# Optimization experiments

Hardware: AMD Instinct MI355X
Metric: run time of the kernel (lower is better)

## Reference

```python
import jax, jax.numpy as jnp
import numpy as np

D_MODEL, D_STATE, EXPAND, HEADDIM = 768, 64, 2, 64
D_INNER = EXPAND * D_MODEL            # 1536
NHEADS = D_INNER // HEADDIM           # 24
D_IN_PROJ = 2 * D_INNER + 2 * D_STATE + 2 * NHEADS  # 3248
DT_MIN, DT_MAX, DT_INIT_FLOOR, A_FLOOR = 1e-3, 1e-1, 1e-4, 1e-4
LN_EPS = 1e-5


def setup_inputs() -> dict:
    key = jax.random.key(0)
    ks = jax.random.split(key, 8)
    B, L = 2, 1024
    u = jax.random.normal(ks[0], (B, L, D_MODEL), dtype=jnp.float32)
    s_in = 1.0 / np.sqrt(D_MODEL)
    s_out = 1.0 / np.sqrt(D_INNER)
    Win = jax.random.uniform(ks[1], (D_IN_PROJ, D_MODEL), jnp.float32, -s_in, s_in)
    Wout = jax.random.uniform(ks[2], (D_MODEL, D_INNER), jnp.float32, -s_out, s_out)
    _dt = jnp.clip(jnp.exp(jax.random.uniform(ks[3], (NHEADS,)) * (np.log(DT_MAX) - np.log(DT_MIN)) + np.log(DT_MIN)), DT_INIT_FLOOR, None)
    dt_bias = _dt + jnp.log(-jnp.expm1(-_dt))
    D = jnp.ones((NHEADS,), jnp.float32)
    Bg = jnp.ones((D_STATE,), jnp.float32)
    Bb = jnp.zeros((D_STATE,), jnp.float32)
    Cg = jnp.ones((D_STATE,), jnp.float32)
    Cb = jnp.zeros((D_STATE,), jnp.float32)
    return {"u": u, "Win": Win, "Wout": Wout, "dt_bias": dt_bias, "D": D,
            "Bg": Bg, "Bb": Bb, "Cg": Cg, "Cb": Cb}


def _layernorm(x, g, b):
    m = jnp.mean(x, axis=-1, keepdims=True)
    v = jnp.var(x, axis=-1, keepdims=True)
    return (x - m) * jax.lax.rsqrt(v + LN_EPS) * g + b


def reference(u, Win, Wout, dt_bias, D, Bg, Bb, Cg, Cb):
    B_, L, _ = u.shape
    nH, hD, dS = NHEADS, HEADDIM, D_STATE
    proj = u @ Win.T  # (B, L, D_IN_PROJ)
    z, x, Bp, Cp, dd_dt, dd_A = jnp.split(
        proj, np.cumsum([D_INNER, D_INNER, dS, dS, nH])[:-0 or None], axis=-1) if False else (
        proj[..., :D_INNER],
        proj[..., D_INNER:2 * D_INNER],
        proj[..., 2 * D_INNER:2 * D_INNER + dS],
        proj[..., 2 * D_INNER + dS:2 * D_INNER + 2 * dS],
        proj[..., 2 * D_INNER + 2 * dS:2 * D_INNER + 2 * dS + nH],
        proj[..., 2 * D_INNER + 2 * dS + nH:])
    x = x.reshape(B_, L, nH, hD)
    z = z.reshape(B_, L, nH, hD)
    Bn = _layernorm(Bp, Bg, Bb)  # (B, L, dS), shared across heads
    Cn = _layernorm(Cp, Cg, Cb)
    DT = jax.nn.softplus(dd_dt + dt_bias)                    # (B, L, nH)
    A = jnp.minimum(-jax.nn.softplus(dd_A), -A_FLOOR)        # (B, L, nH)
    dec = jnp.exp(A * DT)                                    # (B, L, nH)

    def step(h, inp):
        x_t, Bn_t, Cn_t, DT_t, dec_t = inp
        upd = jnp.einsum('bhp,bn->bhpn', x_t, Bn_t) * DT_t[..., None, None]
        h = dec_t[..., None, None] * h + upd
        y_t = jnp.einsum('bhpn,bn->bhp', h, Cn_t) + D[None, :, None] * x_t
        return h, y_t

    h0 = jnp.zeros((B_, nH, hD, dS), u.dtype)
    xs = (jnp.swapaxes(x, 0, 1), jnp.swapaxes(Bn, 0, 1), jnp.swapaxes(Cn, 0, 1),
          jnp.swapaxes(DT, 0, 1), jnp.swapaxes(dec, 0, 1))
    _, ys = jax.lax.scan(step, h0, xs)            # ys: (L, B, nH, hD)
    y = jnp.swapaxes(ys, 0, 1) * jax.nn.silu(z)   # (B, L, nH, hD)
    y = y.reshape(B_, L, D_INNER)
    return y @ Wout.T
```

## Files before the change

kernel.cpp:

```cpp
#include <hip/hip_runtime.h>
#include <cstdint>

#define D_MODEL   768
#define D_STATE   64
#define D_INNER   1536
#define NHEADS    24
#define HEADDIM   64
#define D_PROJ    3248
#define BATCH     2
#define SEQ       1024
#define ROWS      (BATCH*SEQ)
#define LN_EPS    1e-5f
#define A_FLOOR   1e-4f
#define QC        64
#define NCH       (SEQ/QC)
#define LSTR      72

#define RG_U    32
#define RG_WIN  52
#define RG_WO   12
#define KT_1    24
#define KT_2    48

typedef __attribute__((ext_vector_type(8))) short short8;
typedef __attribute__((ext_vector_type(4))) float f32x4;

__device__ __forceinline__ unsigned short f2bf(float f) {
  union { float f; uint32_t u; } v; v.f = f;
  uint32_t r = (v.u + 0x7FFFu + ((v.u >> 16) & 1u)) >> 16;
  return (unsigned short)r;
}
__device__ __forceinline__ float bf2f(unsigned short u) {
  union { uint32_t u; float f; } v; v.u = (uint32_t)u << 16;
  return v.f;
}
__device__ __forceinline__ void storeC(float v, float* p) { *p = v; }
__device__ __forceinline__ void storeC(float v, unsigned short* p) { *p = f2bf(v); }

__device__ __forceinline__ void gload_lds16(const void* g, void* l) {
  __builtin_amdgcn_global_load_lds(
      (const __attribute__((address_space(1))) unsigned int*)g,
      (__attribute__((address_space(3))) unsigned int*)l, 16, 0, 0);
}

template <int N>
__device__ __forceinline__ void wait_vm() {
  static_assert(N == 0 || N == 2 || N == 3 || N == 4 || N == 6 || N == 8,
                "unsupported vmcnt");
  if constexpr (N == 0) asm volatile("s_waitcnt vmcnt(0)" ::: "memory");
  else if constexpr (N == 2) asm volatile("s_waitcnt vmcnt(2)" ::: "memory");
  else if constexpr (N == 3) asm volatile("s_waitcnt vmcnt(3)" ::: "memory");
  else if constexpr (N == 4) asm volatile("s_waitcnt vmcnt(4)" ::: "memory");
  else if constexpr (N == 6) asm volatile("s_waitcnt vmcnt(6)" ::: "memory");
  else if constexpr (N == 8) asm volatile("s_waitcnt vmcnt(8)" ::: "memory");
}

__global__ __launch_bounds__(256) void pack_all_kernel(
    const float* __restrict__ u, const float* __restrict__ Win,
    const float* __restrict__ Wout, unsigned short* __restrict__ upk,
    unsigned short* __restrict__ Winpk, unsigned short* __restrict__ Wopk) {
  int b = blockIdx.x;
  const float* src; unsigned short* dst; int K, RG, kt, rg, srcRows;
  if (b < KT_1 * RG_U) {
    src = u; dst = upk; K = 768; RG = RG_U; kt = b / RG_U; rg = b % RG_U; srcRows = ROWS;
  } else if (b < KT_1 * RG_U + KT_1 * RG_WIN) {
    int i = b - KT_1 * RG_U;
    src = Win; dst = Winpk; K = 768; RG = RG_WIN; kt = i / RG_WIN; rg = i % RG_WIN; srcRows = D_PROJ;
  } else {
    int i = b - KT_1 * RG_U - KT_1 * RG_WIN;
    src = Wout; dst = Wopk; K = 1536; RG = RG_WO; kt = i / RG_WO; rg = i % RG_WO; srcRows = D_MODEL;
  }
  const int t = threadIdx.x;
  const int lr = t >> 2, cq = t & 3;
  const int R = rg * 64 + lr;
  float4 v0 = make_float4(0.f, 0.f, 0.f, 0.f), v1 = v0;
  if (R < srcRows) {
    const float* p = src + (size_t)R * K + kt * 32 + cq * 8;
    v0 = *(const float4*)p;
    v1 = *(const float4*)(p + 4);
  }
  ushort4 oa, ob;
  oa.x = f2bf(v0.x); oa.y = f2bf(v0.y); oa.z = f2bf(v0.z); oa.w = f2bf(v0.w);
  ob.x = f2bf(v1.x); ob.y = f2bf(v1.y); ob.z = f2bf(v1.z); ob.w = f2bf(v1.w);
  unsigned short* o = dst + ((size_t)(kt * RG + rg) * 4 + cq) * 512 + lr * 8;
  *(ushort4*)o = oa;
  *(ushort4*)(o + 4) = ob;
}

template <int TBM, int TBN, int GX, int GY, bool XMAJOR, int SPLIT, typename CT>
__global__ __launch_bounds__(256 * SPLIT) void gemm_bt_bf16(
    const unsigned short* __restrict__ A, const unsigned short* __restrict__ B,
    CT* __restrict__ C, int aRG, int bRG, int M, int N, int K) {
  constexpr int MF = TBM / 32;
  constexpr int NF = TBN / 32;
  constexpr int NSA = TBM / 16;
  constexpr int NSB = TBN / 16;
  constexpr int LPW = (NSA + NSB) / 4;
  static_assert((NSA + NSB) % 4 == 0, "segments must split evenly over waves");
  constexpr int NWG = GX * GY;
  constexpr int PER = NWG / 8;
  static_assert(NWG % 8 == 0, "grid must split evenly over 8 XCDs");
  __shared__ unsigned short Asm[SPLIT][3][TBM * 32];
  __shared__ unsigned short Bsm[SPLIT][3][TBN * 32];

  const int tid = threadIdx.x;
  const int w = tid >> 6, lane = tid & 63;
  const int khalf = w >> 2;
  const int wv = w & 3;
  const int kTiles = (K / SPLIT) >> 5;
  const int ktBase = khalf * kTiles;

  const int g = (blockIdx.x & 7) * PER + (blockIdx.x >> 3);
  int bx, by;
  if constexpr (XMAJOR) { by = g / GX; bx = g - by * GX; }
  else                  { bx = g / GY; by = g - bx * GY; }
  const int bm = by * TBM, bn = bx * TBN;

  const int wm = (wv & 1) * (TBM / 2);
  const int wn = (wv >> 1) * (TBN / 2);
  const int gq = lane >> 4, r = lane & 15;

  f32x4 acc[MF][NF];
#pragma unroll
  for (int i = 0; i < MF; ++i)
#pragma unroll
    for (int j = 0; j < NF; ++j) acc[i][j] = (f32x4){0.f, 0.f, 0.f, 0.f};

  auto stage = [&](int t, int buf) {
    const int kt = ktBase + t;
    for (int s = wv; s < NSA + NSB; s += 4) {
      if (s < NSA) {
        const unsigned short* src =
            A + ((size_t)kt * aRG + (bm >> 6) + (s >> 2)) * 2048 + (s & 3) * 512 + lane * 8;
        gload_lds16(src, (void*)(&Asm[khalf][buf][s * 512]));
      } else {
        int s2 = s - NSA;
        const unsigned short* src =
            B + ((size_t)kt * bRG + (bn >> 6) + (s2 >> 2)) * 2048 + (s2 & 3) * 512 + lane * 8;
        gload_lds16(src, (void*)(&Bsm[khalf][buf][s2 * 512]));
      }
    }
  };

  stage(0, 0);
  stage(1, 1);

  int cur = 0;
  for (int t = 0; t < kTiles; ++t) {
    if (t + 1 < kTiles) wait_vm<LPW>();
    else                wait_vm<0>();
    __builtin_amdgcn_s_barrier();
    asm volatile("" ::: "memory");

    if (t + 2 < kTiles) stage(t + 2, (t + 2) % 3);

    short8 a[MF], b[NF];
#pragma unroll
    for (int mf = 0; mf < MF; ++mf) {
      int ra = wm + mf * 16 + r;
      a[mf] = *(const short8*)&Asm[khalf][cur][(ra >> 6) * 2048 + gq * 512 + (ra & 63) * 8];
    }
#pragma unroll
    for (int nf = 0; nf < NF; ++nf) {
      int rb = wn + nf * 16 + r;
      b[nf] = *(const short8*)&Bsm[khalf][cur][(rb >> 6) * 2048 + gq * 512 + (rb & 63) * 8];
    }
#pragma unroll
    for (int mf = 0; mf < MF; ++mf)
#pragma unroll
      for (int nf = 0; nf < NF; ++nf)
        acc[mf][nf] = __builtin_amdgcn_mfma_f32_16x16x32_bf16(a[mf], b[nf], acc[mf][nf], 0, 0, 0);

    cur = (cur + 1) % 3;
  }

  if constexpr (SPLIT == 2) {
    __syncthreads();
    float* red = (float*)&Asm[0][0][0];
    if (khalf == 1) {
#pragma unroll
      for (int mf = 0; mf < MF; ++mf)
#pragma unroll
        for (int nf = 0; nf < NF; ++nf)
#pragma unroll
          for (int q = 0; q < 4; ++q)
            red[(size_t)wv * 1024 + ((mf * NF + nf) * 4 + q) * 64 + lane] = acc[mf][nf][q];
    }
    __syncthreads();
    if (khalf == 1) return;
#pragma unroll
    for (int mf = 0; mf < MF; ++mf)
#pragma unroll
      for (int nf = 0; nf < NF; ++nf)
#pragma unroll
        for (int q = 0; q < 4; ++q)
          acc[mf][nf][q] += red[(size_t)wv * 1024 + ((mf * NF + nf) * 4 + q) * 64 + lane];
  }

#pragma unroll
  for (int mf = 0; mf < MF; ++mf) {
#pragma unroll
    for (int nf = 0; nf < NF; ++nf) {
      int col = bn + wn + nf * 16 + r;
      if (col < N) {
#pragma unroll
        for (int q = 0; q < 4; ++q) {
          int row = bm + wm + mf * 16 + gq * 4 + q;
          storeC(acc[mf][nf][q], &C[(size_t)row * N + col]);
        }
      }
    }
  }
}

__device__ __forceinline__ float softplusf(float x) {
  return (x > 20.f) ? x : log1pf(expf(x));
}
__device__ __forceinline__ float wave_sum64(float v) {
#pragma unroll
  for (int o = 32; o > 0; o >>= 1) v += __shfl_xor(v, o);
  return v;
}

__global__ __launch_bounds__(256) void prep_kernel(
    const unsigned short* __restrict__ proj, const float* __restrict__ dt_bias,
    const float* __restrict__ Bg, const float* __restrict__ Bb,
    const float* __restrict__ Cg, const float* __restrict__ Cb,
    unsigned short* __restrict__ BC, float2* __restrict__ aDT) {
  const int r = blockIdx.x * 4 + (threadIdx.x >> 6);
  const int lane = threadIdx.x & 63;
  const unsigned short* p = proj + (size_t)r * D_PROJ;

  float bp = bf2f(p[2 * D_INNER + lane]);
  float cp = bf2f(p[2 * D_INNER + D_STATE + lane]);

  float mb = wave_sum64(bp) * (1.f / 64.f);
  float mc = wave_sum64(cp) * (1.f / 64.f);
  float db = bp - mb, dc = cp - mc;
  float vb = wave_sum64(db * db) * (1.f / 64.f);
  float vc = wave_sum64(dc * dc) * (1.f / 64.f);
  float bn = db * rsqrtf(vb + LN_EPS) * Bg[lane] + Bb[lane];
  float cn = dc * rsqrtf(vc + LN_EPS) * Cg[lane] + Cb[lane];
  BC[(size_t)r * 128 + lane]      = f2bf(bn);
  BC[(size_t)r * 128 + 64 + lane] = f2bf(cn);

  if (lane < NHEADS) {
    float ddt = bf2f(p[2 * D_INNER + 2 * D_STATE + lane]);
    float dA  = bf2f(p[2 * D_INNER + 2 * D_STATE + NHEADS + lane]);
    float DT = softplusf(ddt + dt_bias[lane]);
    float Aa = fminf(-softplusf(dA), -A_FLOOR);
    int b = r >> 10;
    int t = r & 1023;
    aDT[((size_t)(b * NHEADS + lane) << 10) + t] = make_float2(Aa * DT, DT);
  }
}

__device__ __forceinline__ float wave_prefix_incl(float v, int lane) {
#pragma unroll
  for (int o = 1; o < 64; o <<= 1) {
    float w = __shfl_up(v, o);
    if (lane >= o) v += w;
  }
  return v;
}

__global__ __launch_bounds__(256) void chunk_state_kernel(
    const unsigned short* __restrict__ proj, const unsigned short* __restrict__ BC,
    const float2* __restrict__ aDT, float* __restrict__ Tbuf,
    float* __restrict__ Ebuf) {
  const int blk = blockIdx.x;
  const int c = blk & (NCH - 1), bh = blk >> 4;
  const int b = bh / NHEADS, hh = bh % NHEADS;
  const int tid = threadIdx.x;

  __shared__ unsigned short BT[64 * LSTR];
  __shared__ unsigned short XT[64 * LSTR];
  __shared__ float coeff[QC];
  __shared__ float etot[1];

  if (tid < 64) {
    float2 ad = aDT[((size_t)bh << 10) + c * QC + tid];
    float cs = wave_prefix_incl(ad.x, tid);
    float tot = __shfl(cs, 63);
    coeff[tid] = ad.y * __expf(tot - cs);
    if (tid == 63) etot[0] = __expf(tot);
  }
  __syncthreads();

  for (int i = tid; i < 1024; i += 256) {
    int s = i >> 4;
    int q = (i & 15) * 4;
    int r = b * SEQ + c * QC + s;
    ushort4 bv = *(const ushort4*)(BC + (size_t)r * 128 + q);
    ushort4 xv = *(const ushort4*)(proj + (size_t)r * D_PROJ + D_INNER + hh * 64 + q);
    float cf = coeff[s];
    BT[(q + 0) * LSTR + s] = bv.x;
    BT[(q + 1) * LSTR + s] = bv.y;
    BT[(q + 2) * LSTR + s] = bv.z;
    BT[(q + 3) * LSTR + s] = bv.w;
    XT[(q + 0) * LSTR + s] = f2bf(bf2f(xv.x) * cf);
    XT[(q + 1) * LSTR + s] = f2bf(bf2f(xv.y) * cf);
    XT[(q + 2) * LSTR + s] = f2bf(bf2f(xv.z) * cf);
    XT[(q + 3) * LSTR + s] = f2bf(bf2f(xv.w) * cf);
  }
  __syncthreads();

  const int w = tid >> 6, l = tid & 63;
  const int r16 = l & 15, g = l >> 4;
  f32x4 acc[4];
#pragma unroll
  for (int i = 0; i < 4; ++i) acc[i] = (f32x4){0.f, 0.f, 0.f, 0.f};

#pragma unroll
  for (int kk = 0; kk < 2; ++kk) {
    short8 a = *(const short8*)&BT[(w * 16 + r16) * LSTR + kk * 32 + g * 8];
#pragma unroll
    for (int pf = 0; pf < 4; ++pf) {
      short8 bf = *(const short8*)&XT[(pf * 16 + r16) * LSTR + kk * 32 + g * 8];
      acc[pf] = __builtin_amdgcn_mfma_f32_16x16x32_bf16(a, bf, acc[pf], 0, 0, 0);
    }
  }

  float* T = Tbuf + (size_t)blk * 4096;
#pragma unroll
  for (int pf = 0; pf < 4; ++pf)
#pragma unroll
    for (int q = 0; q < 4; ++q)
      T[(size_t)(w * 16 + g * 4 + q) * 64 + pf * 16 + r16] = acc[pf][q];
  if (tid == 0) Ebuf[blk] = etot[0];
}

__global__ __launch_bounds__(256) void interchunk_kernel(
    const float* __restrict__ Tbuf, const float* __restrict__ Ebuf,
    float* __restrict__ Sinbuf) {
  const int bh = blockIdx.x >> 2, part = blockIdx.x & 3;
  const int tid = threadIdx.x;
  const size_t eo = (size_t)part * 1024 + tid * 4;
  float4 s = make_float4(0.f, 0.f, 0.f, 0.f);
#pragma unroll
  for (int c = 0; c < NCH; ++c) {
    size_t off = ((size_t)(bh * NCH + c)) * 4096 + eo;
    *(float4*)(Sinbuf + off) = s;
    float E = Ebuf[bh * NCH + c];
    float4 t4 = *(const float4*)(Tbuf + off);
    s.x = fmaf(E, s.x, t4.x);
    s.y = fmaf(E, s.y, t4.y);
    s.z = fmaf(E, s.z, t4.z);
    s.w = fmaf(E, s.w, t4.w);
  }
}

__global__ __launch_bounds__(256) void chunk_output_kernel(
    const unsigned short* __restrict__ proj, const unsigned short* __restrict__ BC,
    const float2* __restrict__ aDT, const float* __restrict__ Sinbuf,
    const float* __restrict__ Dv, unsigned short* __restrict__ Ybf) {
  const int blk = blockIdx.x;
  const int c = blk & (NCH - 1), bh = blk >> 4;
  const int b = bh / NHEADS, hh = bh % NHEADS;
  const int tid = threadIdx.x;

  __shared__ unsigned short Cc[64 * LSTR];
  __shared__ unsigned short Bc[64 * LSTR];
  __shared__ unsigned short SinT[64 * LSTR];
  __shared__ unsigned short XT[64 * LSTR];
  __shared__ unsigned short Wl[64 * LSTR];
  __shared__ float csum[QC];
  __shared__ float DTs[QC];

  if (tid < 64) {
    float2 ad = aDT[((size_t)bh << 10) + c * QC + tid];
    csum[tid] = wave_prefix_incl(ad.x, tid);
    DTs[tid] = ad.y;
  }

  const size_t sin_base = (size_t)blk * 4096;
  for (int i = tid; i < 1024; i += 256) {
    int s = i >> 4;
    int q = (i & 15) * 4;
    int r = b * SEQ + c * QC + s;
    ushort4 bv = *(const ushort4*)(BC + (size_t)r * 128 + q);
    ushort4 cv = *(const ushort4*)(BC + (size_t)r * 128 + 64 + q);
    ushort4 xv = *(const ushort4*)(proj + (size_t)r * D_PROJ + D_INNER + hh * 64 + q);
    float4 sv = *(const float4*)(Sinbuf + sin_base + (size_t)s * 64 + q);
    *(ushort4*)&Cc[s * LSTR + q] = cv;
    *(ushort4*)&Bc[s * LSTR + q] = bv;
    XT[(q + 0) * LSTR + s] = xv.x;
    XT[(q + 1) * LSTR + s] = xv.y;
    XT[(q + 2) * LSTR + s] = xv.z;
    XT[(q + 3) * LSTR + s] = xv.w;
    SinT[(q + 0) * LSTR + s] = f2bf(sv.x);
    SinT[(q + 1) * LSTR + s] = f2bf(sv.y);
    SinT[(q + 2) * LSTR + s] = f2bf(sv.z);
    SinT[(q + 3) * LSTR + s] = f2bf(sv.w);
  }
  __syncthreads();

  const int w = tid >> 6, l = tid & 63;
  const int r16 = l & 15, g = l >> 4;

  f32x4 accg[4], accy[4];
#pragma unroll
  for (int i = 0; i < 4; ++i) {
    accg[i] = (f32x4){0.f, 0.f, 0.f, 0.f};
    accy[i] = (f32x4){0.f, 0.f, 0.f, 0.f};
  }

#pragma unroll
  for (int kk = 0; kk < 2; ++kk) {
    short8 a = *(const short8*)&Cc[(w * 16 + r16) * LSTR + kk * 32 + g * 8];
#pragma unroll
    for (int f = 0; f < 4; ++f) {
      short8 bf = *(const short8*)&Bc[(f * 16 + r16) * LSTR + kk * 32 + g * 8];
      accg[f] = __builtin_amdgcn_mfma_f32_16x16x32_bf16(a, bf, accg[f], 0, 0, 0);
    }
#pragma unroll
    for (int f = 0; f < 4; ++f) {
      short8 bf = *(const short8*)&SinT[(f * 16 + r16) * LSTR + kk * 32 + g * 8];
      accy[f] = __builtin_amdgcn_mfma_f32_16x16x32_bf16(a, bf, accy[f], 0, 0, 0);
    }
  }

  float cst[4], dsc[4];
#pragma unroll
  for (int q = 0; q < 4; ++q) {
    cst[q] = csum[w * 16 + g * 4 + q];
    dsc[q] = __expf(cst[q]);
  }
#pragma unroll
  for (int sf = 0; sf < 4; ++sf) {
    int s = sf * 16 + r16;
    float cs_s = csum[s], dt_s = DTs[s];
#pragma unroll
    for (int q = 0; q < 4; ++q) {
      int t = w * 16 + g * 4 + q;
      float wv = (s <= t) ? accg[sf][q] * __expf(cst[q] - cs_s) * dt_s : 0.f;
      Wl[t * LSTR + s] = f2bf(wv);
    }
  }
#pragma unroll
  for (int f = 0; f < 4; ++f)
#pragma unroll
    for (int q = 0; q < 4; ++q) accy[f][q] *= dsc[q];
  __syncthreads();

#pragma unroll
  for (int kk = 0; kk < 2; ++kk) {
    short8 a = *(const short8*)&Wl[(w * 16 + r16) * LSTR + kk * 32 + g * 8];
#pragma unroll
    for (int f = 0; f < 4; ++f) {
      short8 bf = *(const short8*)&XT[(f * 16 + r16) * LSTR + kk * 32 + g * 8];
      accy[f] = __builtin_amdgcn_mfma_f32_16x16x32_bf16(a, bf, accy[f], 0, 0, 0);
    }
  }

  const float Dh = Dv[hh];
  const int rg = b * 16 + c;
#pragma unroll
  for (int pf = 0; pf < 4; ++pf) {
    int p = pf * 16 + r16;
    int col = hh * 64 + p;
    int kt = col >> 5;
    int cseg = (col >> 3) & 3;
    int jj = p & 7;
    size_t base = ((size_t)(kt * RG_U + rg) * 4 + cseg) * 512 + jj;
#pragma unroll
    for (int q = 0; q < 4; ++q) {
      int t = w * 16 + g * 4 + q;
      int rr = b * SEQ + c * QC + t;
      float x = bf2f(proj[(size_t)rr * D_PROJ + D_INNER + hh * 64 + p]);
      float z = bf2f(proj[(size_t)rr * D_PROJ + hh * 64 + p]);
      float y = accy[pf][q] + Dh * x;
      Ybf[base + (size_t)t * 8] = f2bf(y * (z / (1.f + __expf(-z))));
    }
  }
}

extern "C" void kernel_launch(void* const* d_in, const int* in_sizes, int n_in,
                              void* d_out, int out_size, void* d_ws, size_t ws_size,
                              hipStream_t stream) {
  const float* u       = (const float*)d_in[0];
  const float* Win     = (const float*)d_in[1];
  const float* Wout    = (const float*)d_in[2];
  const float* dt_bias = (const float*)d_in[3];
  const float* Dv      = (const float*)d_in[4];
  const float* Bg      = (const float*)d_in[5];
  const float* Bb      = (const float*)d_in[6];
  const float* Cg      = (const float*)d_in[7];
  const float* Cb      = (const float*)d_in[8];
  float* out = (float*)d_out;

  float* ws = (float*)d_ws;
  unsigned short* projsh = (unsigned short*)ws;
  float*  after_proj = ws + (size_t)ROWS * D_PROJ / 2;
  unsigned short* BCsh = (unsigned short*)after_proj;
  float*  aDTf    = after_proj + (size_t)ROWS * 128 / 2;
  float2* aDT     = (float2*)aDTf;
  float*  Tbuf    = aDTf + (size_t)2 * BATCH * NHEADS * SEQ;
  float*  Ebuf    = Tbuf + (size_t)BATCH * NHEADS * NCH * 4096;
  float*  Sinbuf  = Ebuf + 1024;
  float*  Woutbff = Sinbuf + (size_t)BATCH * NHEADS * NCH * 4096;

  unsigned short* upk   = (unsigned short*)Sinbuf;
  unsigned short* Winpk = (unsigned short*)Tbuf;
  unsigned short* Ypk   = (unsigned short*)Tbuf;
  unsigned short* Wopk  = (unsigned short*)Woutbff;

  pack_all_kernel<<<KT_1 * RG_U + KT_1 * RG_WIN + KT_2 * RG_WO, 256, 0, stream>>>(
      u, Win, Wout, upk, Winpk, Wopk);

  gemm_bt_bf16<128, 128, 26, 16, false, 1, unsigned short><<<416, 256, 0, stream>>>(
      upk, Winpk, projsh, RG_U, RG_WIN, ROWS, D_PROJ, D_MODEL);

  prep_kernel<<<ROWS / 4, 256, 0, stream>>>(projsh, dt_bias, Bg, Bb, Cg, Cb, BCsh, aDT);

  chunk_state_kernel<<<BATCH * NHEADS * NCH, 256, 0, stream>>>(projsh, BCsh, aDT, Tbuf, Ebuf);
  interchunk_kernel<<<BATCH * NHEADS * 4, 256, 0, stream>>>(Tbuf, Ebuf, Sinbuf);
  chunk_output_kernel<<<BATCH * NHEADS * NCH, 256, 0, stream>>>(projsh, BCsh, aDT, Sinbuf, Dv, Ypk);

  gemm_bt_bf16<64, 64, 12, 32, true, 2, float><<<384, 512, 0, stream>>>(
      Ypk, Wopk, out, RG_U, RG_WO, ROWS, D_MODEL, D_INNER);
}
```

Measured before the change: 78.57 us.

## Fuse LayerNorm into GEMM epilogue and merge chunk-state with inter-chunk scan

The B/C LayerNorm moves into the epilogue of the input-projection GEMM, and the separate prep kernel is removed. Chunk-state and inter-chunk kernels merge into one kernel per (batch, head, quarter of headdim) that loops sequentially over chunks, keeps the running state in registers, and prefetches the next chunk's inputs. DT and decay are recomputed from proj in both scan kernels instead of being stored, which removes several launches and intermediate buffers (Tbuf, Ebuf, aDT). In exchange the fused scan runs only 192 blocks with a serial loop over chunks, which lowers parallelism, and the LN uses a single-pass variance.

```diff
diff --git a/kernel.cpp b/kernel.cpp
--- a/kernel.cpp
+++ b/kernel.cpp
@@ -15,6 +15,8 @@
 #define QC        64
 #define NCH       (SEQ/QC)
 #define LSTR      72
+#define COL_DT    3200
+#define COL_DA    3224
 
 #define RG_U    32
 #define RG_WIN  52
@@ -53,6 +55,18 @@
   else if constexpr (N == 4) asm volatile("s_waitcnt vmcnt(4)" ::: "memory");
   else if constexpr (N == 6) asm volatile("s_waitcnt vmcnt(6)" ::: "memory");
   else if constexpr (N == 8) asm volatile("s_waitcnt vmcnt(8)" ::: "memory");
+}
+
+__device__ __forceinline__ float softplusf(float x) {
+  return (x > 20.f) ? x : log1pf(expf(x));
+}
+__device__ __forceinline__ float wave_prefix_incl(float v, int lane) {
+#pragma unroll
+  for (int o = 1; o < 64; o <<= 1) {
+    float w = __shfl_up(v, o);
+    if (lane >= o) v += w;
+  }
+  return v;
 }
 
 __global__ __launch_bounds__(256) void pack_all_kernel(
@@ -87,10 +101,14 @@
   *(ushort4*)(o + 4) = ob;
 }
 
-template <int TBM, int TBN, int GX, int GY, bool XMAJOR, int SPLIT, typename CT>
+template <int TBM, int TBN, int GX, int GY, bool XMAJOR, int SPLIT, bool EPILN,
+          typename CT>
 __global__ __launch_bounds__(256 * SPLIT) void gemm_bt_bf16(
     const unsigned short* __restrict__ A, const unsigned short* __restrict__ B,
-    CT* __restrict__ C, int aRG, int bRG, int M, int N, int K) {
+    CT* __restrict__ C, int aRG, int bRG, int M, int N, int K,
+    const float* __restrict__ LNg0, const float* __restrict__ LNb0,
+    const float* __restrict__ LNg1, const float* __restrict__ LNb1,
+    unsigned short* __restrict__ BCout) {
   constexpr int MF = TBM / 32;
   constexpr int NF = TBN / 32;
   constexpr int NSA = TBM / 16;
@@ -211,148 +229,137 @@
       }
     }
   }
-}
-
-__device__ __forceinline__ float softplusf(float x) {
-  return (x > 20.f) ? x : log1pf(expf(x));
-}
-__device__ __forceinline__ float wave_sum64(float v) {
-#pragma unroll
-  for (int o = 32; o > 0; o >>= 1) v += __shfl_xor(v, o);
-  return v;
-}
-
-__global__ __launch_bounds__(256) void prep_kernel(
-    const unsigned short* __restrict__ proj, const float* __restrict__ dt_bias,
-    const float* __restrict__ Bg, const float* __restrict__ Bb,
-    const float* __restrict__ Cg, const float* __restrict__ Cb,
-    unsigned short* __restrict__ BC, float2* __restrict__ aDT) {
-  const int r = blockIdx.x * 4 + (threadIdx.x >> 6);
-  const int lane = threadIdx.x & 63;
-  const unsigned short* p = proj + (size_t)r * D_PROJ;
-
-  float bp = bf2f(p[2 * D_INNER + lane]);
-  float cp = bf2f(p[2 * D_INNER + D_STATE + lane]);
-
-  float mb = wave_sum64(bp) * (1.f / 64.f);
-  float mc = wave_sum64(cp) * (1.f / 64.f);
-  float db = bp - mb, dc = cp - mc;
-  float vb = wave_sum64(db * db) * (1.f / 64.f);
-  float vc = wave_sum64(dc * dc) * (1.f / 64.f);
-  float bn = db * rsqrtf(vb + LN_EPS) * Bg[lane] + Bb[lane];
-  float cn = dc * rsqrtf(vc + LN_EPS) * Cg[lane] + Cb[lane];
-  BC[(size_t)r * 128 + lane]      = f2bf(bn);
-  BC[(size_t)r * 128 + 64 + lane] = f2bf(cn);
-
-  if (lane < NHEADS) {
-    float ddt = bf2f(p[2 * D_INNER + 2 * D_STATE + lane]);
-    float dA  = bf2f(p[2 * D_INNER + 2 * D_STATE + NHEADS + lane]);
-    float DT = softplusf(ddt + dt_bias[lane]);
-    float Aa = fminf(-softplusf(dA), -A_FLOOR);
-    int b = r >> 10;
-    int t = r & 1023;
-    aDT[((size_t)(b * NHEADS + lane) << 10) + t] = make_float2(Aa * DT, DT);
-  }
-}
-
-__device__ __forceinline__ float wave_prefix_incl(float v, int lane) {
-#pragma unroll
-  for (int o = 1; o < 64; o <<= 1) {
-    float w = __shfl_up(v, o);
-    if (lane >= o) v += w;
-  }
-  return v;
-}
-
-__global__ __launch_bounds__(256) void chunk_state_kernel(
+
+  if constexpr (EPILN) {
+    if (bn == 2 * D_INNER) {
+      const float* gma = (wn == 0) ? LNg0 : LNg1;
+      const float* bta = (wn == 0) ? LNb0 : LNb1;
+      const int half = (wn == 0) ? 0 : 64;
+#pragma unroll
+      for (int mf = 0; mf < MF; ++mf) {
+#pragma unroll
+        for (int q = 0; q < 4; ++q) {
+          float s1 = 0.f, s2 = 0.f;
+#pragma unroll
+          for (int nf = 0; nf < NF; ++nf) {
+            float v = acc[mf][nf][q];
+            s1 += v; s2 += v * v;
+          }
+#pragma unroll
+          for (int o = 1; o < 16; o <<= 1) {
+            s1 += __shfl_xor(s1, o);
+            s2 += __shfl_xor(s2, o);
+          }
+          float mean = s1 * (1.f / 64.f);
+          float var = s2 * (1.f / 64.f) - mean * mean;
+          float rs = rsqrtf(fmaxf(var, 0.f) + LN_EPS);
+          int row = bm + wm + mf * 16 + gq * 4 + q;
+#pragma unroll
+          for (int nf = 0; nf < NF; ++nf) {
+            int n = nf * 16 + r;
+            BCout[(size_t)row * 128 + half + n] =
+                f2bf((acc[mf][nf][q] - mean) * rs * gma[n] + bta[n]);
+          }
+        }
+      }
+    }
+  }
+}
+
+__global__ __launch_bounds__(256) void scan_fused_kernel(
     const unsigned short* __restrict__ proj, const unsigned short* __restrict__ BC,
-    const float2* __restrict__ aDT, float* __restrict__ Tbuf,
-    float* __restrict__ Ebuf) {
-  const int blk = blockIdx.x;
-  const int c = blk & (NCH - 1), bh = blk >> 4;
+    const float* __restrict__ dt_bias, float* __restrict__ Sinbuf) {
+  const int part = blockIdx.x & 3, bh = blockIdx.x >> 2;
   const int b = bh / NHEADS, hh = bh % NHEADS;
+  const int p0 = part * 16;
   const int tid = threadIdx.x;
+  const int w = tid >> 6, l = tid & 63, r16 = l & 15, g = l >> 4;
 
   __shared__ unsigned short BT[64 * LSTR];
-  __shared__ unsigned short XT[64 * LSTR];
-  __shared__ float coeff[QC];
-  __shared__ float etot[1];
-
-  if (tid < 64) {
-    float2 ad = aDT[((size_t)bh << 10) + c * QC + tid];
-    float cs = wave_prefix_incl(ad.x, tid);
-    float tot = __shfl(cs, 63);
-    coeff[tid] = ad.y * __expf(tot - cs);
-    if (tid == 63) etot[0] = __expf(tot);
+  __shared__ unsigned short XT[16 * LSTR];
+  __shared__ float coeffA[NCH][QC];
+  __shared__ float etotA[NCH];
+
+  {
+    const float dtb = dt_bias[hh];
+#pragma unroll
+    for (int j = 0; j < 4; ++j) {
+      int c = w + j * 4;
+      int rr = b * SEQ + c * QC + l;
+      float ddt = bf2f(proj[(size_t)rr * D_PROJ + COL_DT + hh]);
+      float dA  = bf2f(proj[(size_t)rr * D_PROJ + COL_DA + hh]);
+      float DT = softplusf(ddt + dtb);
+      float Aa = fminf(-softplusf(dA), -A_FLOOR);
+      float cs = wave_prefix_incl(Aa * DT, l);
+      float tot = __shfl(cs, 63);
+      coeffA[c][l] = DT * __expf(tot - cs);
+      if (l == 63) etotA[c] = __expf(tot);
+    }
   }
   __syncthreads();
 
-  for (int i = tid; i < 1024; i += 256) {
-    int s = i >> 4;
-    int q = (i & 15) * 4;
-    int r = b * SEQ + c * QC + s;
-    ushort4 bv = *(const ushort4*)(BC + (size_t)r * 128 + q);
-    ushort4 xv = *(const ushort4*)(proj + (size_t)r * D_PROJ + D_INNER + hh * 64 + q);
-    float cf = coeff[s];
-    BT[(q + 0) * LSTR + s] = bv.x;
-    BT[(q + 1) * LSTR + s] = bv.y;
-    BT[(q + 2) * LSTR + s] = bv.z;
-    BT[(q + 3) * LSTR + s] = bv.w;
-    XT[(q + 0) * LSTR + s] = f2bf(bf2f(xv.x) * cf);
-    XT[(q + 1) * LSTR + s] = f2bf(bf2f(xv.y) * cf);
-    XT[(q + 2) * LSTR + s] = f2bf(bf2f(xv.z) * cf);
-    XT[(q + 3) * LSTR + s] = f2bf(bf2f(xv.w) * cf);
-  }
-  __syncthreads();
-
-  const int w = tid >> 6, l = tid & 63;
-  const int r16 = l & 15, g = l >> 4;
-  f32x4 acc[4];
-#pragma unroll
-  for (int i = 0; i < 4; ++i) acc[i] = (f32x4){0.f, 0.f, 0.f, 0.f};
-
-#pragma unroll
-  for (int kk = 0; kk < 2; ++kk) {
-    short8 a = *(const short8*)&BT[(w * 16 + r16) * LSTR + kk * 32 + g * 8];
-#pragma unroll
-    for (int pf = 0; pf < 4; ++pf) {
-      short8 bf = *(const short8*)&XT[(pf * 16 + r16) * LSTR + kk * 32 + g * 8];
-      acc[pf] = __builtin_amdgcn_mfma_f32_16x16x32_bf16(a, bf, acc[pf], 0, 0, 0);
-    }
-  }
-
-  float* T = Tbuf + (size_t)blk * 4096;
-#pragma unroll
-  for (int pf = 0; pf < 4; ++pf)
-#pragma unroll
-    for (int q = 0; q < 4; ++q)
-      T[(size_t)(w * 16 + g * 4 + q) * 64 + pf * 16 + r16] = acc[pf][q];
-  if (tid == 0) Ebuf[blk] = etot[0];
-}
-
-__global__ __launch_bounds__(256) void interchunk_kernel(
-    const float* __restrict__ Tbuf, const float* __restrict__ Ebuf,
-    float* __restrict__ Sinbuf) {
-  const int bh = blockIdx.x >> 2, part = blockIdx.x & 3;
-  const int tid = threadIdx.x;
-  const size_t eo = (size_t)part * 1024 + tid * 4;
-  float4 s = make_float4(0.f, 0.f, 0.f, 0.f);
-#pragma unroll
+  ushort4 rB[4];
+  ushort4 rX;
+  auto loadRegs = [&](int c) {
+#pragma unroll
+    for (int j = 0; j < 4; ++j) {
+      int i = tid + j * 256;
+      int s = i >> 4, q = (i & 15) * 4;
+      rB[j] = *(const ushort4*)(BC + (size_t)(b * SEQ + c * QC + s) * 128 + q);
+    }
+    int s = tid >> 2, pq = (tid & 3) * 4;
+    rX = *(const ushort4*)(proj + (size_t)(b * SEQ + c * QC + s) * D_PROJ +
+                           D_INNER + hh * 64 + p0 + pq);
+  };
+
+  loadRegs(0);
+  f32x4 S = (f32x4){0.f, 0.f, 0.f, 0.f};
+
   for (int c = 0; c < NCH; ++c) {
-    size_t off = ((size_t)(bh * NCH + c)) * 4096 + eo;
-    *(float4*)(Sinbuf + off) = s;
-    float E = Ebuf[bh * NCH + c];
-    float4 t4 = *(const float4*)(Tbuf + off);
-    s.x = fmaf(E, s.x, t4.x);
-    s.y = fmaf(E, s.y, t4.y);
-    s.z = fmaf(E, s.z, t4.z);
-    s.w = fmaf(E, s.w, t4.w);
+#pragma unroll
+    for (int j = 0; j < 4; ++j) {
+      int i = tid + j * 256;
+      int s = i >> 4, q = (i & 15) * 4;
+      float cf = coeffA[c][s];
+      BT[(q + 0) * LSTR + s] = f2bf(bf2f(rB[j].x) * cf);
+      BT[(q + 1) * LSTR + s] = f2bf(bf2f(rB[j].y) * cf);
+      BT[(q + 2) * LSTR + s] = f2bf(bf2f(rB[j].z) * cf);
+      BT[(q + 3) * LSTR + s] = f2bf(bf2f(rB[j].w) * cf);
+    }
+    {
+      int s = tid >> 2, pq = (tid & 3) * 4;
+      XT[(pq + 0) * LSTR + s] = rX.x;
+      XT[(pq + 1) * LSTR + s] = rX.y;
+      XT[(pq + 2) * LSTR + s] = rX.z;
+      XT[(pq + 3) * LSTR + s] = rX.w;
+    }
+    __syncthreads();
+
+    if (c + 1 < NCH) loadRegs(c + 1);
+
+    f32x4 T = (f32x4){0.f, 0.f, 0.f, 0.f};
+#pragma unroll
+    for (int kk = 0; kk < 2; ++kk) {
+      short8 a = *(const short8*)&BT[(w * 16 + r16) * LSTR + kk * 32 + g * 8];
+      short8 bf = *(const short8*)&XT[r16 * LSTR + kk * 32 + g * 8];
+      T = __builtin_amdgcn_mfma_f32_16x16x32_bf16(a, bf, T, 0, 0, 0);
+    }
+
+    const float E = etotA[c];
+    size_t base = (size_t)(bh * NCH + c) * 4096;
+#pragma unroll
+    for (int q = 0; q < 4; ++q) {
+      int n = w * 16 + g * 4 + q;
+      Sinbuf[base + (size_t)n * 64 + p0 + r16] = S[q];
+      S[q] = fmaf(E, S[q], T[q]);
+    }
+    __syncthreads();
   }
 }
 
 __global__ __launch_bounds__(256) void chunk_output_kernel(
     const unsigned short* __restrict__ proj, const unsigned short* __restrict__ BC,
-    const float2* __restrict__ aDT, const float* __restrict__ Sinbuf,
+    const float* __restrict__ dt_bias, const float* __restrict__ Sinbuf,
     const float* __restrict__ Dv, unsigned short* __restrict__ Ybf) {
   const int blk = blockIdx.x;
   const int c = blk & (NCH - 1), bh = blk >> 4;
@@ -368,9 +375,13 @@
   __shared__ float DTs[QC];
 
   if (tid < 64) {
-    float2 ad = aDT[((size_t)bh << 10) + c * QC + tid];
-    csum[tid] = wave_prefix_incl(ad.x, tid);
-    DTs[tid] = ad.y;
+    int rr = b * SEQ + c * QC + tid;
+    float ddt = bf2f(proj[(size_t)rr * D_PROJ + COL_DT + hh]);
+    float dA  = bf2f(proj[(size_t)rr * D_PROJ + COL_DA + hh]);
+    float DT = softplusf(ddt + dt_bias[hh]);
+    float Aa = fminf(-softplusf(dA), -A_FLOOR);
+    csum[tid] = wave_prefix_incl(Aa * DT, tid);
+    DTs[tid] = DT;
   }
 
   const size_t sin_base = (size_t)blk * 4096;
@@ -491,32 +502,32 @@
 
   float* ws = (float*)d_ws;
   unsigned short* projsh = (unsigned short*)ws;
-  float*  after_proj = ws + (size_t)ROWS * D_PROJ / 2;
+  float* after_proj = ws + (size_t)ROWS * D_PROJ / 2;
   unsigned short* BCsh = (unsigned short*)after_proj;
-  float*  aDTf    = after_proj + (size_t)ROWS * 128 / 2;
-  float2* aDT     = (float2*)aDTf;
-  float*  Tbuf    = aDTf + (size_t)2 * BATCH * NHEADS * SEQ;
-  float*  Ebuf    = Tbuf + (size_t)BATCH * NHEADS * NCH * 4096;
-  float*  Sinbuf  = Ebuf + 1024;
-  float*  Woutbff = Sinbuf + (size_t)BATCH * NHEADS * NCH * 4096;
+  float* regionA = after_proj + (size_t)ROWS * 128 / 2;
+  float* Sinbuf  = regionA + 1600000;
+  float* WopkF   = Sinbuf + (size_t)BATCH * NHEADS * NCH * 4096;
 
   unsigned short* upk   = (unsigned short*)Sinbuf;
-  unsigned short* Winpk = (unsigned short*)Tbuf;
-  unsigned short* Ypk   = (unsigned short*)Tbuf;
-  unsigned short* Wopk  = (unsigned short*)Woutbff;
+  unsigned short* Winpk = (unsigned short*)regionA;
+  unsigned short* Ypk   = (unsigned short*)regionA;
+  unsigned short* Wopk  = (unsigned short*)WopkF;
 
   pack_all_kernel<<<KT_1 * RG_U + KT_1 * RG_WIN + KT_2 * RG_WO, 256, 0, stream>>>(
       u, Win, Wout, upk, Winpk, Wopk);
 
-  gemm_bt_bf16<128, 128, 26, 16, false, 1, unsigned short><<<416, 256, 0, stream>>>(
-      upk, Winpk, projsh, RG_U, RG_WIN, ROWS, D_PROJ, D_MODEL);
-
-  prep_kernel<<<ROWS / 4, 256, 0, stream>>>(projsh, dt_bias, Bg, Bb, Cg, Cb, BCsh, aDT);
-
-  chunk_state_kernel<<<BATCH * NHEADS * NCH, 256, 0, stream>>>(projsh, BCsh, aDT, Tbuf, Ebuf);
-  interchunk_kernel<<<BATCH * NHEADS * 4, 256, 0, stream>>>(Tbuf, Ebuf, Sinbuf);
-  chunk_output_kernel<<<BATCH * NHEADS * NCH, 256, 0, stream>>>(projsh, BCsh, aDT, Sinbuf, Dv, Ypk);
-
-  gemm_bt_bf16<64, 64, 12, 32, true, 2, float><<<384, 512, 0, stream>>>(
-      Ypk, Wopk, out, RG_U, RG_WO, ROWS, D_MODEL, D_INNER);
-}
+  gemm_bt_bf16<128, 128, 26, 16, false, 1, true, unsigned short>
+      <<<416, 256, 0, stream>>>(upk, Winpk, projsh, RG_U, RG_WIN,
+                                ROWS, D_PROJ, D_MODEL, Bg, Bb, Cg, Cb, BCsh);
+
+  scan_fused_kernel<<<BATCH * NHEADS * 4, 256, 0, stream>>>(
+      projsh, BCsh, dt_bias, Sinbuf);
+
+  chunk_output_kernel<<<BATCH * NHEADS * NCH, 256, 0, stream>>>(
+      projsh, BCsh, dt_bias, Sinbuf, Dv, Ypk);
+
+  gemm_bt_bf16<64, 64, 12, 32, true, 2, false, float>
+      <<<384, 512, 0, stream>>>(Ypk, Wopk, out, RG_U, RG_WO,
+                                ROWS, D_MODEL, D_INNER,
+                                nullptr, nullptr, nullptr, nullptr, nullptr);
+}
```

Measured after the change: 87.91 us. 11.9% more time.
